# Performance work log

Hardware: AMD Instinct MI355X
Metric: run time of the kernel (lower is better)

## Reference

```python
import jax, jax.numpy as jnp
import numpy as np

def setup_inputs() -> dict:
    key = jax.random.key(0)
    ks = jax.random.split(key, 8)
    B, n, in_dim, h = 4, 512, 300, 128
    word_vecs = jax.random.normal(ks[0], (B, n, in_dim), dtype=jnp.float32)
    mask = jnp.zeros((B, n, h), dtype=jnp.float32)
    s_in = 1.0 / np.sqrt(in_dim)
    s_h = 1.0 / np.sqrt(h)
    Wx_w = jax.random.normal(ks[1], (h, in_dim), dtype=jnp.float32) * s_in
    Wx_b = jnp.zeros((h,), dtype=jnp.float32)
    Wa_w = jax.random.normal(ks[2], (h, h), dtype=jnp.float32) * s_h
    Wa_b = jnp.zeros((h,), dtype=jnp.float32)
    Ua_w = jax.random.normal(ks[3], (h, h), dtype=jnp.float32) * s_h
    Ua_b = jnp.zeros((h,), dtype=jnp.float32)
    return {"word_vecs": word_vecs, "mask": mask, "Wx_w": Wx_w, "Wx_b": Wx_b,
            "Wa_w": Wa_w, "Wa_b": Wa_b, "Ua_w": Ua_w, "Ua_b": Ua_b}

def reference(word_vecs, mask, Wx_w, Wx_b, Wa_w, Wa_b, Ua_w, Ua_b):
    # h_vecs: [B, n, h]  (dropout layers are identity in eval mode)
    h_vecs = jnp.tanh(jnp.einsum('bni,hi->bnh', word_vecs, Wx_w) + Wx_b)
    ta = jnp.einsum('bnh,gh->bng', h_vecs, Wa_w) + Wa_b  # [B,n,h]
    tb = jnp.einsum('bnh,gh->bng', h_vecs, Ua_w) + Ua_b  # [B,n,h]
    # additive per-channel scores: [B, q, k, h]
    temp = jax.nn.elu(ta[:, :, None, :] + tb[:, None, :, :])
    a = jax.nn.softmax(temp + mask[:, None, :, :], axis=2)
    # weighted sum over keys: [B, q, h]
    c_vecs = jnp.einsum('bqkh,bkh->bqh', a, h_vecs)
    return c_vecs
```

## Files before the change

kernel.cpp:

```cpp
#include <hip/hip_runtime.h>

#define B_    4
#define N_    512
#define IND_  300
#define H_    128
#define QQ    4
#define KC    8
#define LOG2E 1.4426950408889634f

__global__ void pack_wx(const float* __restrict__ w, float* __restrict__ dst) {
    const int i = blockIdx.x;
    const int t = threadIdx.x;
    dst[(i >> 2) * 512 + t * 4 + (i & 3)] = w[t * IND_ + i];
}

__global__ void pack_sq(const float* __restrict__ w, float* __restrict__ dst, float scale) {
    const int i = blockIdx.x;
    const int t = threadIdx.x;
    dst[(i >> 2) * 512 + t * 4 + (i & 3)] = w[t * H_ + i] * scale;
}

__global__ void scale_mask(const float* __restrict__ m, float* __restrict__ dst) {
    const int idx = blockIdx.x * 256 + threadIdx.x;
    dst[idx] = m[idx] * LOG2E;
}

__global__ __launch_bounds__(128) void prep2(
    const float* __restrict__ x,
    const float* __restrict__ WxT4,
    const float* __restrict__ Wx_b,
    const float* __restrict__ WaT4,
    const float* __restrict__ Wa_b,
    const float* __restrict__ UaT4,
    const float* __restrict__ Ua_b,
    float2* __restrict__ pairs,
    float* __restrict__ taS)
{
    __shared__ __align__(16) float xs[304];
    __shared__ __align__(16) float hs[H_];

    const int r = blockIdx.x;
    const int t = threadIdx.x;

    const float* xrow = x + (size_t)r * IND_;
    for (int i = t; i < IND_; i += 128) xs[i] = xrow[i];
    __syncthreads();

    const float4* w4 = (const float4*)WxT4 + t;
    float acc = Wx_b[t];
    #pragma unroll 5
    for (int i4 = 0; i4 < IND_ / 4; ++i4) {
        float4 w  = w4[i4 * 128];
        float4 xv = *(const float4*)(xs + 4 * i4);
        acc = fmaf(w.x, xv.x, acc);
        acc = fmaf(w.y, xv.y, acc);
        acc = fmaf(w.z, xv.z, acc);
        acc = fmaf(w.w, xv.w, acc);
    }
    float h = tanhf(acc);
    hs[t] = h;
    __syncthreads();

    const float4* wa4 = (const float4*)WaT4 + t;
    const float4* ua4 = (const float4*)UaT4 + t;
    float accA = Wa_b[t] * LOG2E;
    float accU = Ua_b[t] * LOG2E;
    #pragma unroll 8
    for (int i4 = 0; i4 < H_ / 4; ++i4) {
        float4 wa = wa4[i4 * 128];
        float4 ua = ua4[i4 * 128];
        float4 hv = *(const float4*)(hs + 4 * i4);
        accA = fmaf(wa.x, hv.x, accA);
        accA = fmaf(wa.y, hv.y, accA);
        accA = fmaf(wa.z, hv.z, accA);
        accA = fmaf(wa.w, hv.w, accA);
        accU = fmaf(ua.x, hv.x, accU);
        accU = fmaf(ua.y, hv.y, accU);
        accU = fmaf(ua.z, hv.z, accU);
        accU = fmaf(ua.w, hv.w, accU);
    }
    taS[(size_t)r * H_ + t]   = accA;
    pairs[(size_t)r * H_ + t] = make_float2(accU, h);
}

__global__ __launch_bounds__(128) void attn2(
    const float* __restrict__ taS,
    const float2* __restrict__ pairs,
    const float* __restrict__ mkS,
    float* __restrict__ accum)
{
    const int c  = blockIdx.x;
    const int qg = blockIdx.y;
    const int b  = blockIdx.z;
    const int h  = threadIdx.x;
    const int q0 = qg * QQ;
    const int kstep = N_ / KC;

    float taq[QQ], l[QQ], cc[QQ];
    #pragma unroll
    for (int j = 0; j < QQ; ++j) {
        taq[j] = taS[((size_t)(b * N_ + q0 + j)) * H_ + h];
        l[j] = 0.f;
        cc[j] = 0.f;
    }

    const float2* pb = pairs + ((size_t)b * N_ + c * kstep) * H_ + h;
    const float*  mb = mkS   + ((size_t)b * N_ + c * kstep) * H_ + h;

    #pragma unroll 4
    for (int k = 0; k < kstep; ++k) {
        float2 tv   = pb[(size_t)k * H_];
        float  mkL  = mb[(size_t)k * H_];
        float  mkmL = mkL - LOG2E;
        #pragma unroll
        for (int j = 0; j < QQ; ++j) {
            float x    = taq[j] + tv.x;
            float e    = __builtin_amdgcn_exp2f(x);
            float argP = x + mkL;
            float argN = fmaf(e, LOG2E, mkmL);
            float arg  = (x > 0.f) ? argP : argN;
            float p    = __builtin_amdgcn_exp2f(arg);
            l[j] += p;
            cc[j] = fmaf(p, tv.y, cc[j]);
        }
    }

    #pragma unroll
    for (int j = 0; j < QQ; ++j) {
        size_t base = ((size_t)(b * N_ + q0 + j)) * H_ + h;
        atomicAdd(&accum[base * 2],     l[j]);
        atomicAdd(&accum[base * 2 + 1], cc[j]);
    }
}

__global__ void fin_kernel(const float2* __restrict__ accum, float* __restrict__ out) {
    const int idx = blockIdx.x * 256 + threadIdx.x;
    float2 a = accum[idx];
    out[idx] = a.y / a.x;
}

extern "C" void kernel_launch(void* const* d_in, const int* in_sizes, int n_in,
                              void* d_out, int out_size, void* d_ws, size_t ws_size,
                              hipStream_t stream) {
    const float* word_vecs = (const float*)d_in[0];
    const float* mask      = (const float*)d_in[1];
    const float* Wx_w      = (const float*)d_in[2];
    const float* Wx_b      = (const float*)d_in[3];
    const float* Wa_w      = (const float*)d_in[4];
    const float* Wa_b      = (const float*)d_in[5];
    const float* Ua_w      = (const float*)d_in[6];
    const float* Ua_b      = (const float*)d_in[7];
    float* out = (float*)d_out;

    char* p = (char*)d_ws;
    float*  WxT4  = (float*)p;              p += (size_t)75 * 512 * 4;
    float*  WaT4  = (float*)p;              p += (size_t)32 * 512 * 4;
    float*  UaT4  = (float*)p;              p += (size_t)32 * 512 * 4;
    float*  taS   = (float*)p;              p += (size_t)B_ * N_ * H_ * 4;
    float2* pairs = (float2*)p;             p += (size_t)B_ * N_ * H_ * 8;
    float*  mkS   = (float*)p;              p += (size_t)B_ * N_ * H_ * 4;
    float*  accum = (float*)p;              p += (size_t)B_ * N_ * H_ * 8;

    hipMemsetAsync(accum, 0, (size_t)B_ * N_ * H_ * 8, stream);

    pack_wx<<<IND_, 128, 0, stream>>>(Wx_w, WxT4);
    pack_sq<<<H_, 128, 0, stream>>>(Wa_w, WaT4, LOG2E);
    pack_sq<<<H_, 128, 0, stream>>>(Ua_w, UaT4, LOG2E);
    scale_mask<<<(B_ * N_ * H_) / 256, 256, 0, stream>>>(mask, mkS);

    prep2<<<B_ * N_, 128, 0, stream>>>(word_vecs, WxT4, Wx_b,
                                       WaT4, Wa_b, UaT4, Ua_b, pairs, taS);

    dim3 grid(KC, N_ / QQ, B_);
    attn2<<<grid, 128, 0, stream>>>(taS, pairs, mkS, accum);

    fin_kernel<<<(B_ * N_ * H_) / 256, 256, 0, stream>>>((const float2*)accum, out);
}
```

Baseline: 143.2 us.

## Factor exponentials out of the pairwise loop and replace atomics with partial buffers

Precomputes exp2 of the query and key projections and of the mask in the prep kernel. This way the pairwise ELU-softmax term needs one exp2 and a few multiplies, where it needed two exp2 per (q,k,h) before. Each key row is packed as a float4 (exp of the key projection, exp of the mask, h). Per-chunk partial sums go to separate buffers that a final kernel reduces, instead of using atomics on a memset buffer. The queries per block go from 4 to 8, and the weight-pack and mask kernels are merged or dropped. The risks are overflow of the exponential products for large activations and a larger partial-sum workspace.

```diff
diff --git a/kernel.cpp b/kernel.cpp
--- a/kernel.cpp
+++ b/kernel.cpp
@@ -4,28 +4,31 @@
 #define N_    512
 #define IND_  300
 #define H_    128
-#define QQ    4
+#define QQ    8
 #define KC    8
 #define LOG2E 1.4426950408889634f
 
-__global__ void pack_wx(const float* __restrict__ w, float* __restrict__ dst) {
-    const int i = blockIdx.x;
-    const int t = threadIdx.x;
-    dst[(i >> 2) * 512 + t * 4 + (i & 3)] = w[t * IND_ + i];
+__global__ void pack_all(const float* __restrict__ Wx_w,
+                         const float* __restrict__ Wa_w,
+                         const float* __restrict__ Ua_w,
+                         float* __restrict__ WxT4,
+                         float* __restrict__ WaT4,
+                         float* __restrict__ UaT4) {
+    const int blk = blockIdx.x;
+    const int t   = threadIdx.x;
+    if (blk < IND_) {
+        const int i = blk;
+        WxT4[(i >> 2) * 512 + t * 4 + (i & 3)] = Wx_w[t * IND_ + i];
+    } else if (blk < IND_ + H_) {
+        const int i = blk - IND_;
+        WaT4[(i >> 2) * 512 + t * 4 + (i & 3)] = Wa_w[t * H_ + i] * LOG2E;
+    } else {
+        const int i = blk - IND_ - H_;
+        UaT4[(i >> 2) * 512 + t * 4 + (i & 3)] = Ua_w[t * H_ + i] * LOG2E;
+    }
 }
 
-__global__ void pack_sq(const float* __restrict__ w, float* __restrict__ dst, float scale) {
-    const int i = blockIdx.x;
-    const int t = threadIdx.x;
-    dst[(i >> 2) * 512 + t * 4 + (i & 3)] = w[t * H_ + i] * scale;
-}
-
-__global__ void scale_mask(const float* __restrict__ m, float* __restrict__ dst) {
-    const int idx = blockIdx.x * 256 + threadIdx.x;
-    dst[idx] = m[idx] * LOG2E;
-}
-
-__global__ __launch_bounds__(128) void prep2(
+__global__ __launch_bounds__(128) void prep3(
     const float* __restrict__ x,
     const float* __restrict__ WxT4,
     const float* __restrict__ Wx_b,
@@ -33,8 +36,9 @@
     const float* __restrict__ Wa_b,
     const float* __restrict__ UaT4,
     const float* __restrict__ Ua_b,
-    float2* __restrict__ pairs,
-    float* __restrict__ taS)
+    const float* __restrict__ mask,
+    float* __restrict__ Eta,
+    float4* __restrict__ kv)
 {
     __shared__ __align__(16) float xs[304];
     __shared__ __align__(16) float hs[H_];
@@ -79,64 +83,65 @@
         accU = fmaf(ua.z, hv.z, accU);
         accU = fmaf(ua.w, hv.w, accU);
     }
-    taS[(size_t)r * H_ + t]   = accA;
-    pairs[(size_t)r * H_ + t] = make_float2(accU, h);
+    const size_t o = (size_t)r * H_ + t;
+    Eta[o] = __builtin_amdgcn_exp2f(accA);
+    float M = __builtin_amdgcn_exp2f(mask[o] * LOG2E);
+    kv[o]  = make_float4(__builtin_amdgcn_exp2f(accU), M, h, 0.f);
 }
 
-__global__ __launch_bounds__(128) void attn2(
-    const float* __restrict__ taS,
-    const float2* __restrict__ pairs,
-    const float* __restrict__ mkS,
-    float* __restrict__ accum)
+__global__ __launch_bounds__(128) void attn3(
+    const float* __restrict__ Eta,
+    const float4* __restrict__ kv,
+    float2* __restrict__ accum)
 {
     const int c  = blockIdx.x;
     const int qg = blockIdx.y;
     const int b  = blockIdx.z;
     const int h  = threadIdx.x;
     const int q0 = qg * QQ;
-    const int kstep = N_ / KC;
+    const int k0 = c * (N_ / KC);
 
-    float taq[QQ], l[QQ], cc[QQ];
+    float eta[QQ], l[QQ], cc[QQ];
     #pragma unroll
     for (int j = 0; j < QQ; ++j) {
-        taq[j] = taS[((size_t)(b * N_ + q0 + j)) * H_ + h];
+        eta[j] = Eta[((size_t)(b * N_ + q0 + j)) * H_ + h];
         l[j] = 0.f;
         cc[j] = 0.f;
     }
 
-    const float2* pb = pairs + ((size_t)b * N_ + c * kstep) * H_ + h;
-    const float*  mb = mkS   + ((size_t)b * N_ + c * kstep) * H_ + h;
+    const float4* kp = kv + ((size_t)(b * N_ + k0)) * H_ + h;
 
     #pragma unroll 4
-    for (int k = 0; k < kstep; ++k) {
-        float2 tv   = pb[(size_t)k * H_];
-        float  mkL  = mb[(size_t)k * H_];
-        float  mkmL = mkL - LOG2E;
+    for (int k = 0; k < N_ / KC; ++k) {
+        float4 v = kp[(size_t)k * H_];
         #pragma unroll
         for (int j = 0; j < QQ; ++j) {
-            float x    = taq[j] + tv.x;
-            float e    = __builtin_amdgcn_exp2f(x);
-            float argP = x + mkL;
-            float argN = fmaf(e, LOG2E, mkmL);
-            float arg  = (x > 0.f) ? argP : argN;
-            float p    = __builtin_amdgcn_exp2f(arg);
+            float e  = eta[j] * v.x;
+            float pn = __builtin_amdgcn_exp2f(fmaf(e, LOG2E, -LOG2E));
+            float p0 = (e > 1.f) ? e : pn;
+            float p  = p0 * v.y;
             l[j] += p;
-            cc[j] = fmaf(p, tv.y, cc[j]);
+            cc[j] = fmaf(p, v.z, cc[j]);
         }
     }
 
     #pragma unroll
     for (int j = 0; j < QQ; ++j) {
-        size_t base = ((size_t)(b * N_ + q0 + j)) * H_ + h;
-        atomicAdd(&accum[base * 2],     l[j]);
-        atomicAdd(&accum[base * 2 + 1], cc[j]);
+        accum[((size_t)c * (B_ * N_) + b * N_ + q0 + j) * H_ + h] =
+            make_float2(l[j], cc[j]);
     }
 }
 
-__global__ void fin_kernel(const float2* __restrict__ accum, float* __restrict__ out) {
+__global__ void fin3(const float2* __restrict__ accum, float* __restrict__ out) {
     const int idx = blockIdx.x * 256 + threadIdx.x;
-    float2 a = accum[idx];
-    out[idx] = a.y / a.x;
+    float L = 0.f, C = 0.f;
+    #pragma unroll
+    for (int c = 0; c < KC; ++c) {
+        float2 a = accum[(size_t)c * (B_ * N_ * H_) + idx];
+        L += a.x;
+        C += a.y;
+    }
+    out[idx] = C / L;
 }
 
 extern "C" void kernel_launch(void* const* d_in, const int* in_sizes, int n_in,
@@ -153,26 +158,21 @@
     float* out = (float*)d_out;
 
     char* p = (char*)d_ws;
-    float*  WxT4  = (float*)p;              p += (size_t)75 * 512 * 4;
-    float*  WaT4  = (float*)p;              p += (size_t)32 * 512 * 4;
-    float*  UaT4  = (float*)p;              p += (size_t)32 * 512 * 4;
-    float*  taS   = (float*)p;              p += (size_t)B_ * N_ * H_ * 4;
-    float2* pairs = (float2*)p;             p += (size_t)B_ * N_ * H_ * 8;
-    float*  mkS   = (float*)p;              p += (size_t)B_ * N_ * H_ * 4;
-    float*  accum = (float*)p;              p += (size_t)B_ * N_ * H_ * 8;
+    float*  WxT4  = (float*)p;   p += (size_t)75 * 512 * 4;
+    float*  WaT4  = (float*)p;   p += (size_t)32 * 512 * 4;
+    float*  UaT4  = (float*)p;   p += (size_t)32 * 512 * 4;
+    float*  Eta   = (float*)p;   p += (size_t)B_ * N_ * H_ * 4;
+    float4* kv    = (float4*)p;  p += (size_t)B_ * N_ * H_ * 16;
+    float2* accum = (float2*)p;  p += (size_t)KC * B_ * N_ * H_ * 8;
 
-    hipMemsetAsync(accum, 0, (size_t)B_ * N_ * H_ * 8, stream);
+    pack_all<<<IND_ + 2 * H_, 128, 0, stream>>>(Wx_w, Wa_w, Ua_w, WxT4, WaT4, UaT4);
 
-    pack_wx<<<IND_, 128, 0, stream>>>(Wx_w, WxT4);
-    pack_sq<<<H_, 128, 0, stream>>>(Wa_w, WaT4, LOG2E);
-    pack_sq<<<H_, 128, 0, stream>>>(Ua_w, UaT4, LOG2E);
-    scale_mask<<<(B_ * N_ * H_) / 256, 256, 0, stream>>>(mask, mkS);
-
-    prep2<<<B_ * N_, 128, 0, stream>>>(word_vecs, WxT4, Wx_b,
-                                       WaT4, Wa_b, UaT4, Ua_b, pairs, taS);
+    prep3<<<B_ * N_, 128, 0, stream>>>(word_vecs, WxT4, Wx_b,
+                                       WaT4, Wa_b, UaT4, Ua_b,
+                                       mask, Eta, kv);
 
     dim3 grid(KC, N_ / QQ, B_);
-    attn2<<<grid, 128, 0, stream>>>(taS, pairs, mkS, accum);
+    attn3<<<grid, 128, 0, stream>>>(Eta, kv, accum);
 
-    fin_kernel<<<(B_ * N_ * H_) / 256, 256, 0, stream>>>((const float2*)accum, out);
+    fin3<<<(B_ * N_ * H_) / 256, 256, 0, stream>>>(accum, out);
 }
```

Result: faster. 131.4 us (-8.2%).
